# Performance work log

Hardware: AMD Instinct MI355X
Metric: run time of the kernel (lower is better)

The kernel has to match this reference:

```python
import jax, jax.numpy as jnp
import numpy as np

DIM = 1024
HEADS = 16
DH = 64            # dim // heads
LOCAL_HEADS = 8
WINDOW = 128
NEG = -jnp.finfo(jnp.float32).max


def _look_around_kv(z, pad_value):
    # z: (b, h, nw, w, d) -> (b, h, nw, 3w, d); backward=1, forward=1 window
    nw = z.shape[2]
    zp = jnp.pad(z, ((0, 0), (0, 0), (1, 1), (0, 0), (0, 0)), constant_values=pad_value)
    return jnp.concatenate([zp[:, :, i:i + nw] for i in range(3)], axis=3)


def _local_attention(q, k, v, valid):
    # q,k,v: (b, h, t, d); valid: (b, t) True = keep (module passes ~input_mask)
    b, h, t, d = q.shape
    nw = t // WINDOW
    bucket = lambda z: z.reshape(b, h, nw, WINDOW, d)
    bq, bk, bv = bucket(q), bucket(k), bucket(v)
    bk = _look_around_kv(bk, 0.0)
    bv = _look_around_kv(bv, 0.0)
    # key position indices with -1 padding for out-of-range windows
    t_idx = jnp.arange(t, dtype=jnp.int32).reshape(nw, WINDOW)
    tp = jnp.pad(t_idx, ((1, 1), (0, 0)), constant_values=-1)
    bq_k = jnp.concatenate([tp[i:i + nw] for i in range(3)], axis=1)  # (nw, 3w)
    oob = (bq_k == -1)[None, None, :, None, :]                        # (1,1,nw,1,3w)
    # input mask pair: mq & mk
    vm = valid.reshape(b, nw, WINDOW)
    vmp = jnp.pad(vm, ((0, 0), (1, 1), (0, 0)), constant_values=False)
    vmk = jnp.concatenate([vmp[:, i:i + nw] for i in range(3)], axis=2)  # (b, nw, 3w)
    pair = vm[:, None, :, :, None] & vmk[:, None, :, None, :]            # (b,1,nw,w,3w)
    dots = jnp.einsum('bhnwd,bhnkd->bhnwk', bq, bk) * (d ** -0.5)
    dots = jnp.where(oob, NEG, dots)
    dots = jnp.where(pair, dots, NEG)
    attn = jax.nn.softmax(dots, axis=-1)
    out = jnp.einsum('bhnwk,bhnkd->bhnwd', attn, bv)
    return out.reshape(b, h, t, d)


def _linear_attn(q, k, v, valid):
    # q,k,v: (b, h, t, d); valid: (b, t) True = keep
    d = q.shape[-1]
    m = valid[:, None, :, None]
    k = jnp.where(m, k, NEG)
    v = jnp.where(m, v, 0.0)
    q = jax.nn.softmax(q, axis=-1) * (d ** -0.5)
    k = jax.nn.softmax(k, axis=-2)
    context = jnp.einsum('bhnd,bhne->bhde', k, v)
    return jnp.einsum('bhnd,bhde->bhne', q, context)


def setup_inputs() -> dict:
    key = jax.random.key(0)
    ks = jax.random.split(key, 7)
    b, t = 2, 4096
    x = jax.random.normal(ks[0], (b, t, DIM), dtype=jnp.float32)
    input_mask = jax.random.bernoulli(ks[1], 0.1, (b, t))  # True = padded token
    s = DIM ** -0.5
    Wq = jax.random.normal(ks[2], (DIM, HEADS * DH), jnp.float32) * s
    Wk = jax.random.normal(ks[3], (DIM, HEADS * DH), jnp.float32) * s
    Wv = jax.random.normal(ks[4], (DIM, HEADS * DH), jnp.float32) * s
    Wo = jax.random.normal(ks[5], (HEADS * DH, DIM), jnp.float32) * s
    bo = jax.random.normal(ks[6], (DIM,), jnp.float32) * 0.01
    return {"x": x, "input_mask": input_mask, "Wq": Wq, "Wk": Wk, "Wv": Wv, "Wo": Wo, "bo": bo}


def reference(x, input_mask, Wq, Wk, Wv, Wo, bo):
    b, t, _ = x.shape
    split_heads = lambda z: z.reshape(b, t, HEADS, DH).transpose(0, 2, 1, 3)
    q = split_heads(x @ Wq)
    k = split_heads(x @ Wk)
    v = split_heads(x @ Wv)
    valid = ~input_mask
    lq, gq = q[:, :LOCAL_HEADS], q[:, LOCAL_HEADS:]
    lk, gk = k[:, :LOCAL_HEADS], k[:, LOCAL_HEADS:]
    lv, gv = v[:, :LOCAL_HEADS], v[:, LOCAL_HEADS:]
    local_out = _local_attention(lq, lk, lv, valid)
    global_out = _linear_attn(gq, gk, gv, valid)
    attn = jnp.concatenate([local_out, global_out], axis=1)  # (b, h, t, d)
    attn = attn.transpose(0, 2, 1, 3).reshape(b, t, HEADS * DH)
    return attn @ Wo + bo
```

## Files before the change

### kernel.cpp

```cpp
#include <hip/hip_runtime.h>
#include <cstdint>
#include <cfloat>
#include <math.h>

typedef __bf16 bf16_t;
typedef __bf16 bf16x8 __attribute__((ext_vector_type(8)));
typedef __bf16 bf16x4 __attribute__((ext_vector_type(4)));
typedef float  f32x4  __attribute__((ext_vector_type(4)));
typedef unsigned int u32;

#define NEGF (-3.4028234663852886e38f)

static __device__ __forceinline__ f32x4 mfma16(bf16x8 a, bf16x8 b, f32x4 c) {
  return __builtin_amdgcn_mfma_f32_16x16x32_bf16(a, b, c, 0, 0, 0);
}
static __device__ __forceinline__ void gload_lds16(const bf16_t* g, bf16_t* l) {
  __builtin_amdgcn_global_load_lds((const __attribute__((address_space(1))) void*)g,
                                   (__attribute__((address_space(3))) void*)l, 16, 0, 0);
}

__global__ __launch_bounds__(256) void k_prep_all(const float* __restrict__ x,
                                                  const uint8_t* __restrict__ mraw,
                                                  const float* __restrict__ Wq,
                                                  const float* __restrict__ Wk,
                                                  const float* __restrict__ Wv,
                                                  const float* __restrict__ Wo,
                                                  bf16_t* __restrict__ xb,
                                                  bf16_t* __restrict__ WT,
                                                  bf16_t* __restrict__ WoT,
                                                  uint8_t* __restrict__ valid) {
  int bid = blockIdx.x;
  int tid = threadIdx.x;
  if (bid < 8192) {
    int i = bid * 256 + tid;
    float4 v = ((const float4*)x)[i];
    bf16x4 o = { (bf16_t)v.x, (bf16_t)v.y, (bf16_t)v.z, (bf16_t)v.w };
    *(bf16x4*)(xb + (size_t)i * 4) = o;
  } else if (bid < 12288) {
    __shared__ float tile[32][33];
    int zz = bid - 8192;
    int z = zz >> 10, rem = zz & 1023;
    int bx = rem & 31, by = rem >> 5;
    const float* src = (z == 0) ? Wq : (z == 1) ? Wk : (z == 2) ? Wv : Wo;
    bf16_t* dst = (z < 3) ? (WT + (size_t)z * 1024 * 1024) : WoT;
    int x0 = bx * 32, y0 = by * 32;
    int tx = tid & 31, ty = tid >> 5;
    #pragma unroll
    for (int j = 0; j < 32; j += 8)
      tile[ty + j][tx] = src[(size_t)(y0 + ty + j) * 1024 + x0 + tx];
    __syncthreads();
    #pragma unroll
    for (int j = 0; j < 32; j += 8)
      dst[(size_t)(x0 + ty + j) * 1024 + y0 + tx] = (bf16_t)tile[tx][ty + j];
  } else {
    __shared__ int f1, f3;
    if (tid == 0) { f1 = 0; f3 = 0; }
    __syncthreads();
    int l1 = 0, l3 = 0;
    for (int i = tid; i < 8192; i += 256) {
      uint8_t v = mraw[i];
      if (v) { int r = i & 3; if (r == 1 || r == 2) l1 = 1; if (r == 3) l3 = 1; }
    }
    if (l1) atomicOr(&f1, 1);
    if (l3) atomicOr(&f3, 1);
    __syncthreads();
    int layout = f1 ? 0 : (f3 ? 2 : 1);
    for (int i = tid; i < 8192; i += 256) {
      bool m;
      if (layout == 0)      m = mraw[i] != 0;
      else if (layout == 1) m = ((const int*)mraw)[i] != 0;
      else                  m = ((const float*)mraw)[i] != 0.0f;
      valid[i] = m ? (uint8_t)0 : (uint8_t)1;
    }
  }
}

template<bool OUT_BF16>
__global__ __launch_bounds__(256, 2) void k_gemm(const bf16_t* __restrict__ A,
                                                 const bf16_t* __restrict__ Bt,
                                                 void* __restrict__ Cout,
                                                 const float* __restrict__ bias,
                                                 int M, int N, int K) {
  __shared__ __align__(16) uint8_t shmem[34816];
  bf16_t* As = (bf16_t*)shmem;
  bf16_t* Bs = As + 128 * 64;
  int id  = blockIdx.x;
  int seq = id >> 3;
  int nbg = seq >> 6, inner = seq & 63;
  int mb = ((id & 7) << 3) + (inner >> 3);
  int nb = (nbg << 3) + (inner & 7);

  const int tid = threadIdx.x;
  const int lane = tid & 63, wv = tid >> 6;
  const int c = lane & 15, g = lane >> 4;
  const size_t m0 = (size_t)mb * 128, n0 = (size_t)nb * 128;
  const int wm = (wv >> 1) * 64, wn = (wv & 1) * 64;

  f32x4 zero = {0.f, 0.f, 0.f, 0.f};
  f32x4 acc[4][4];
  #pragma unroll
  for (int m = 0; m < 4; ++m)
    #pragma unroll
    for (int n = 0; n < 4; ++n) acc[m][n] = zero;

  for (int kt = 0; kt < K; kt += 64) {
    if (kt) __syncthreads();
    #pragma unroll
    for (int p = 0; p < 4; ++p) {
      int seg = p * 256 + tid;
      int r = seg >> 3, s = seg & 7;
      int sc = (s ^ (r & 7)) * 8;
      gload_lds16(A + (m0 + r) * (size_t)K + kt + sc, As + seg * 8);
    }
    #pragma unroll
    for (int p = 0; p < 4; ++p) {
      int seg = p * 256 + tid;
      int r = seg >> 3, s = seg & 7;
      int sc = (s ^ (r & 7)) * 8;
      gload_lds16(Bt + (n0 + r) * (size_t)K + kt + sc, Bs + seg * 8);
    }
    __syncthreads();
    #pragma unroll
    for (int kk = 0; kk < 2; ++kk) {
      bf16x8 af[4], bfv[4];
      #pragma unroll
      for (int m = 0; m < 4; ++m) {
        int row = wm + m * 16 + c;
        int sl = (g + 4 * kk) ^ (row & 7);
        af[m] = *(const bf16x8*)(As + row * 64 + sl * 8);
      }
      #pragma unroll
      for (int n = 0; n < 4; ++n) {
        int row = wn + n * 16 + c;
        int sl = (g + 4 * kk) ^ (row & 7);
        bfv[n] = *(const bf16x8*)(Bs + row * 64 + sl * 8);
      }
      #pragma unroll
      for (int m = 0; m < 4; ++m)
        #pragma unroll
        for (int n = 0; n < 4; ++n)
          acc[m][n] = mfma16(af[m], bfv[n], acc[m][n]);
    }
  }

  __syncthreads();
  if (OUT_BF16) {
    bf16_t* L = (bf16_t*)shmem;
    #pragma unroll
    for (int m = 0; m < 4; ++m)
      #pragma unroll
      for (int n = 0; n < 4; ++n)
        #pragma unroll
        for (int i = 0; i < 4; ++i)
          L[(wm + m * 16 + 4 * g + i) * 136 + wn + n * 16 + c] = (bf16_t)acc[m][n][i];
    __syncthreads();
    bf16_t* C = (bf16_t*)Cout;
    #pragma unroll
    for (int p = 0; p < 8; ++p) {
      int idx = p * 2048 + tid * 8;
      int row = idx >> 7, col = idx & 127;
      bf16x8 v = *(const bf16x8*)(L + row * 136 + col);
      *(bf16x8*)(C + (m0 + row) * (size_t)N + n0 + col) = v;
    }
  } else {
    float* C = (float*)Cout;
    float* L = (float*)shmem;
    #pragma unroll
    for (int half = 0; half < 2; ++half) {
      if (half) __syncthreads();
      if ((wv >> 1) == half) {
        #pragma unroll
        for (int m = 0; m < 4; ++m)
          #pragma unroll
          for (int n = 0; n < 4; ++n)
            #pragma unroll
            for (int i = 0; i < 4; ++i)
              L[(m * 16 + 4 * g + i) * 132 + wn + n * 16 + c] = acc[m][n][i];
      }
      __syncthreads();
      #pragma unroll
      for (int p = 0; p < 8; ++p) {
        int lin = p * 1024 + tid * 4;
        int row = lin >> 7, col = lin & 127;
        float4 v = *(const float4*)(L + row * 132 + col);
        float4 bv = *(const float4*)(bias + n0 + col);
        v.x += bv.x; v.y += bv.y; v.z += bv.z; v.w += bv.w;
        *(float4*)(C + (m0 + half * 64 + row) * (size_t)N + n0 + col) = v;
      }
    }
  }
}

__global__ __launch_bounds__(512) void k_attn(const bf16_t* __restrict__ qkv,
                                              const uint8_t* __restrict__ valid,
                                              bf16_t* __restrict__ attn,
                                              float* __restrict__ ctxp,
                                              float* __restrict__ sump) {
  __shared__ __align__(16) uint8_t smem[50688];
  int bid = blockIdx.x;
  int tid = threadIdx.x;
  const int lane = tid & 63, wv = tid >> 6;
  const int c = lane & 15, g = lane >> 4;
  f32x4 zero = {0.f, 0.f, 0.f, 0.f};

  if (bid < 512) {
    bf16_t* Ks = (bf16_t*)smem;
    bf16_t* VT = (bf16_t*)smem;
    uint8_t* s_key = smem + 50176;
    uint8_t* s_q   = smem + 50560;

    int w = bid & 31, h = (bid >> 5) & 7, b = bid >> 8;
    const int tkbase = (w - 1) * 128;

    #pragma unroll
    for (int p = 0; p < 6; ++p) {
      int seg = p * 512 + tid;
      int r = seg >> 3, s = seg & 7;
      int tk = tkbase + r;
      bf16x8 v8 = { (bf16_t)0.f,(bf16_t)0.f,(bf16_t)0.f,(bf16_t)0.f,
                    (bf16_t)0.f,(bf16_t)0.f,(bf16_t)0.f,(bf16_t)0.f };
      if ((unsigned)tk < 4096u)
        v8 = *(const bf16x8*)(qkv + (size_t)(b * 4096 + tk) * 3072 + 1024 + h * 64 + s * 8);
      *(bf16x8*)(Ks + r * 64 + ((s ^ (r & 7)) * 8)) = v8;
    }
    if (tid < 384) {
      int tk = tkbase + tid;
      s_key[tid] = ((unsigned)tk < 4096u) ? valid[b * 4096 + tk] : (uint8_t)0;
    }
    if (tid < 128) s_q[tid] = valid[b * 4096 + w * 128 + tid];
    __syncthreads();

    int m0 = wv * 16;
    bf16x8 qa0, qa1;
    {
      const bf16_t* qrow = qkv + (size_t)(b * 4096 + w * 128 + m0 + c) * 3072 + h * 64;
      qa0 = *(const bf16x8*)(qrow + g * 8);
      qa1 = *(const bf16x8*)(qrow + 32 + g * 8);
    }
    f32x4 acc[24];
    #pragma unroll
    for (int nt = 0; nt < 24; ++nt) acc[nt] = zero;
    #pragma unroll
    for (int nt = 0; nt < 24; ++nt) {
      int n = nt * 16 + c;
      bf16x8 k0 = *(const bf16x8*)(Ks + n * 64 + ((g       ^ (n & 7)) * 8));
      bf16x8 k1 = *(const bf16x8*)(Ks + n * 64 + (((g + 4) ^ (n & 7)) * 8));
      acc[nt] = mfma16(k0, qa0, acc[nt]);
      acc[nt] = mfma16(k1, qa1, acc[nt]);
    }
    __syncthreads();

    #pragma unroll
    for (int p = 0; p < 6; ++p) {
      int seg = p * 512 + tid;
      int r = seg >> 3, s = seg & 7;
      int tk = tkbase + r;
      bf16x8 v8 = { (bf16_t)0.f,(bf16_t)0.f,(bf16_t)0.f,(bf16_t)0.f,
                    (bf16_t)0.f,(bf16_t)0.f,(bf16_t)0.f,(bf16_t)0.f };
      if ((unsigned)tk < 4096u)
        v8 = *(const bf16x8*)(qkv + (size_t)(b * 4096 + tk) * 3072 + 2048 + h * 64 + s * 8);
      #pragma unroll
      for (int j = 0; j < 8; ++j)
        VT[(s * 8 + j) * 392 + r] = v8[j];
    }

    bool qv = s_q[m0 + c] != 0;
    #pragma unroll
    for (int nt = 0; nt < 24; ++nt) {
      u32 kv4 = *(const u32*)(s_key + nt * 16 + 4 * g);
      #pragma unroll
      for (int i = 0; i < 4; ++i) {
        bool kv = ((kv4 >> (8 * i)) & 255u) != 0u;
        acc[nt][i] = (qv && kv) ? acc[nt][i] * 0.125f : NEGF;
      }
    }
    float mx = NEGF;
    #pragma unroll
    for (int nt = 0; nt < 24; ++nt)
      #pragma unroll
      for (int i = 0; i < 4; ++i) mx = fmaxf(mx, acc[nt][i]);
    mx = fmaxf(mx, __shfl_xor(mx, 16, 64));
    mx = fmaxf(mx, __shfl_xor(mx, 32, 64));

    const int srcA = ((lane >> 4) & 1) * 32 + (lane & 15);
    const int srcB = srcA + 16;
    union Pk2 { bf16x4 h; uint2 u; };
    union Pk4 { uint4 u; bf16x8 h; };
    uint4 paU[12];
    #pragma unroll
    for (int ks = 0; ks < 12; ++ks) paU[ks] = make_uint4(0, 0, 0, 0);
    float sum = 0.f;
    #pragma unroll
    for (int nt = 0; nt < 24; ++nt) {
      Pk2 pk;
      #pragma unroll
      for (int i = 0; i < 4; ++i) {
        float e = __expf(acc[nt][i] - mx);
        sum += e;
        pk.h[i] = (bf16_t)e;
      }
      u32 a0 = (u32)__shfl((int)pk.u.x, srcA, 64);
      u32 a1 = (u32)__shfl((int)pk.u.y, srcA, 64);
      u32 b0 = (u32)__shfl((int)pk.u.x, srcB, 64);
      u32 b1 = (u32)__shfl((int)pk.u.y, srcB, 64);
      bool take = ((g >> 1) == (nt & 1));
      int ks = nt >> 1;
      paU[ks].x = take ? a0 : paU[ks].x;
      paU[ks].y = take ? a1 : paU[ks].y;
      paU[ks].z = take ? b0 : paU[ks].z;
      paU[ks].w = take ? b1 : paU[ks].w;
    }
    sum += __shfl_xor(sum, 16, 64);
    sum += __shfl_xor(sum, 32, 64);
    float inv = 1.f / sum;
    float invq[4];
    #pragma unroll
    for (int i = 0; i < 4; ++i) invq[i] = __shfl(inv, 4 * g + i, 64);
    __syncthreads();

    f32x4 o[4];
    #pragma unroll
    for (int n = 0; n < 4; ++n) o[n] = zero;
    #pragma unroll
    for (int ks = 0; ks < 12; ++ks) {
      Pk4 pa; pa.u = paU[ks];
      #pragma unroll
      for (int n = 0; n < 4; ++n) {
        bf16x8 vb = *(const bf16x8*)(VT + (n * 16 + c) * 392 + ks * 32 + g * 8);
        o[n] = mfma16(pa.h, vb, o[n]);
      }
    }
    size_t obase = (size_t)(b * 4096 + w * 128 + m0) * 1024 + h * 64;
    #pragma unroll
    for (int n = 0; n < 4; ++n)
      #pragma unroll
      for (int i = 0; i < 4; ++i)
        attn[obase + (size_t)(4 * g + i) * 1024 + n * 16 + c] = (bf16_t)(o[n][i] * invq[i]);
  } else {
    int bid2 = bid - 512;
    int tc = bid2 & 15, h = (bid2 >> 4) & 7, b = bid2 >> 7;
    bf16_t* eKT = (bf16_t*)smem;
    bf16_t* vT  = (bf16_t*)(smem + 17408);
    int dt = wv >> 1, et2 = (wv & 1) * 2;
    f32x4 acc2[2];
    acc2[0] = zero; acc2[1] = zero;
    float rowsum = 0.f;
    int rsrow = wv * 8 + (lane >> 3);
    int rscol = (lane & 7) * 16;
    for (int ch = 0; ch < 2; ++ch) {
      __syncthreads();
      #pragma unroll
      for (int p = 0; p < 2; ++p) {
        int idx = p * 512 + tid;
        int r = idx >> 3, ss = idx & 7;
        int gt = b * 4096 + tc * 256 + ch * 128 + r;
        bool vld = valid[gt] != 0;
        bf16x8 k8 = *(const bf16x8*)(qkv + (size_t)gt * 3072 + 1024 + (8 + h) * 64 + ss * 8);
        bf16x8 v8 = *(const bf16x8*)(qkv + (size_t)gt * 3072 + 2048 + (8 + h) * 64 + ss * 8);
        #pragma unroll
        for (int j = 0; j < 8; ++j) {
          int dd = ss * 8 + j;
          eKT[dd * 136 + r] = vld ? (bf16_t)__expf((float)k8[j]) : (bf16_t)0.f;
          vT [dd * 136 + r] = vld ? v8[j] : (bf16_t)0.f;
        }
      }
      __syncthreads();
      #pragma unroll
      for (int ks = 0; ks < 4; ++ks) {
        bf16x8 af = *(const bf16x8*)(eKT + (dt * 16 + c) * 136 + ks * 32 + g * 8);
        #pragma unroll
        for (int n = 0; n < 2; ++n) {
          bf16x8 bf = *(const bf16x8*)(vT + ((et2 + n) * 16 + c) * 136 + ks * 32 + g * 8);
          acc2[n] = mfma16(af, bf, acc2[n]);
        }
      }
      float s = 0.f;
      #pragma unroll
      for (int q = 0; q < 2; ++q) {
        bf16x8 e8 = *(const bf16x8*)(eKT + rsrow * 136 + rscol + q * 8);
        #pragma unroll
        for (int j = 0; j < 8; ++j) s += (float)e8[j];
      }
      rowsum += s;
    }
    rowsum += __shfl_xor(rowsum, 1, 64);
    rowsum += __shfl_xor(rowsum, 2, 64);
    rowsum += __shfl_xor(rowsum, 4, 64);
    size_t slice = (size_t)((b * 8 + h) * 16 + tc);
    #pragma unroll
    for (int n = 0; n < 2; ++n)
      #pragma unroll
      for (int i = 0; i < 4; ++i)
        ctxp[slice * 4096 + (size_t)(dt * 16 + 4 * g + i) * 64 + (et2 + n) * 16 + c] = acc2[n][i];
    if ((lane & 7) == 0)
      sump[slice * 64 + rsrow] = rowsum;
  }
}

__global__ __launch_bounds__(256) void k_ctx2(const float* __restrict__ ctxp,
                                              const float* __restrict__ sump,
                                              bf16_t* __restrict__ ctxT) {
  int bh = blockIdx.x;
  int tid = threadIdx.x;
  __shared__ float inv[64];
  if (tid < 64) {
    float s = 0.f;
    #pragma unroll
    for (int tc = 0; tc < 16; ++tc)
      s += sump[(size_t)(bh * 16 + tc) * 64 + tid];
    inv[tid] = 1.f / s;
  }
  __syncthreads();
  for (int p = 0; p < 16; ++p) {
    int lin = p * 256 + tid;
    int d = lin >> 6, e = lin & 63;
    float s = 0.f;
    #pragma unroll
    for (int tc = 0; tc < 16; ++tc)
      s += ctxp[(size_t)(bh * 16 + tc) * 4096 + lin];
    s *= inv[d];
    ctxT[(size_t)bh * 4096 + e * 64 + d] = (bf16_t)s;
  }
}

__global__ __launch_bounds__(256) void k_linout(const bf16_t* __restrict__ qkv,
                                                const bf16_t* __restrict__ ctxT,
                                                bf16_t* __restrict__ attn) {
  int bid = blockIdx.x;
  int tb2 = bid & 15, hg = (bid >> 4) & 7, b = bid >> 7;
  int tid = threadIdx.x;
  __shared__ bf16_t qs[256 * 72];
  __shared__ bf16_t cT[64 * 72];
  {
    int t = tb2 * 256 + tid;
    const bf16_t* qrow = qkv + (size_t)(b * 4096 + t) * 3072 + (8 + hg) * 64;
    float x[64];
    #pragma unroll
    for (int s8 = 0; s8 < 8; ++s8) {
      bf16x8 q8 = *(const bf16x8*)(qrow + s8 * 8);
      #pragma unroll
      for (int j = 0; j < 8; ++j) x[s8 * 8 + j] = (float)q8[j];
    }
    float m = x[0];
    #pragma unroll
    for (int i = 1; i < 64; ++i) m = fmaxf(m, x[i]);
    float sum = 0.f;
    #pragma unroll
    for (int i = 0; i < 64; ++i) { x[i] = __expf(x[i] - m); sum += x[i]; }
    float sc = 0.125f / sum;
    #pragma unroll
    for (int s8 = 0; s8 < 8; ++s8) {
      bf16x8 o8;
      #pragma unroll
      for (int j = 0; j < 8; ++j) o8[j] = (bf16_t)(x[s8 * 8 + j] * sc);
      *(bf16x8*)(qs + tid * 72 + s8 * 8) = o8;
    }
  }
  for (int idx = tid; idx < 512; idx += 256) {
    int r = idx >> 3, s = idx & 7;
    *(bf16x8*)(cT + r * 72 + s * 8) =
      *(const bf16x8*)(ctxT + (size_t)(b * 8 + hg) * 4096 + r * 64 + s * 8);
  }
  __syncthreads();
  int lane = tid & 63, wvv = tid >> 6;
  int c = lane & 15, g = lane >> 4;
  int m0w = wvv * 64;
  f32x4 zero = {0.f, 0.f, 0.f, 0.f};
  f32x4 acc[4][4];
  #pragma unroll
  for (int m = 0; m < 4; ++m)
    #pragma unroll
    for (int n = 0; n < 4; ++n) acc[m][n] = zero;
  #pragma unroll
  for (int kk = 0; kk < 2; ++kk) {
    bf16x8 af[4], bfv[4];
    #pragma unroll
    for (int m = 0; m < 4; ++m)
      af[m] = *(const bf16x8*)(qs + (m0w + m * 16 + c) * 72 + kk * 32 + g * 8);
    #pragma unroll
    for (int n = 0; n < 4; ++n)
      bfv[n] = *(const bf16x8*)(cT + (n * 16 + c) * 72 + kk * 32 + g * 8);
    #pragma unroll
    for (int m = 0; m < 4; ++m)
      #pragma unroll
      for (int n = 0; n < 4; ++n)
        acc[m][n] = mfma16(af[m], bfv[n], acc[m][n]);
  }
  size_t obase = (size_t)(b * 4096 + tb2 * 256 + m0w) * 1024 + (8 + hg) * 64;
  #pragma unroll
  for (int m = 0; m < 4; ++m)
    #pragma unroll
    for (int n = 0; n < 4; ++n)
      #pragma unroll
      for (int i = 0; i < 4; ++i)
        attn[obase + (size_t)(m * 16 + 4 * g + i) * 1024 + n * 16 + c] = (bf16_t)acc[m][n][i];
}

extern "C" void kernel_launch(void* const* d_in, const int* in_sizes, int n_in,
                              void* d_out, int out_size, void* d_ws, size_t ws_size,
                              hipStream_t stream) {
  const float*   x    = (const float*)d_in[0];
  const uint8_t* mraw = (const uint8_t*)d_in[1];
  const float*   Wq   = (const float*)d_in[2];
  const float*   Wk   = (const float*)d_in[3];
  const float*   Wv   = (const float*)d_in[4];
  const float*   Wo   = (const float*)d_in[5];
  const float*   bo   = (const float*)d_in[6];
  uint8_t* ws = (uint8_t*)d_ws;

  uint8_t* valid = ws;
  bf16_t*  xb    = (bf16_t*)(ws + 8192);
  bf16_t*  WT    = (bf16_t*)(ws + 16785408);
  bf16_t*  WoT   = (bf16_t*)(ws + 23076864);
  bf16_t*  qkv   = (bf16_t*)(ws + 25174016);
  bf16_t*  attn  = (bf16_t*)(ws + 75505664);
  float*   ctxp  = (float*)(ws + 8192);
  float*   sump  = (float*)(ws + 4202496);
  bf16_t*  ctxT  = (bf16_t*)(ws + 4268032);

  k_prep_all<<<12289, 256, 0, stream>>>(x, mraw, Wq, Wk, Wv, Wo, xb, WT, WoT, valid);
  k_gemm<true><<<1536, 256, 0, stream>>>(xb, WT, (void*)qkv, nullptr, 8192, 3072, 1024);
  k_attn<<<768, 512, 0, stream>>>(qkv, valid, attn, ctxp, sump);
  k_ctx2<<<16, 256, 0, stream>>>(ctxp, sump, ctxT);
  k_linout<<<256, 256, 0, stream>>>(qkv, ctxT, attn);
  k_gemm<false><<<512, 256, 0, stream>>>(attn, WoT, d_out, bo, 8192, 1024, 1024);
}
```

Before: 177.0 us.

## Overlap K/V global loads with compute via direct-to-LDS and register prefetch

In the local-attention blocks, K is now staged with direct global-to-LDS loads in the same XOR-swizzled layout. V is loaded into registers during the QK^T/softmax phase and only transposed into LDS after softmax, which removes a barrier. In the linear-attention blocks, the two-chunk loop is unrolled so the second chunk's K/V global loads are issued before the first chunk's MFMA work. The K load drops the bounds check, so edge windows read rows outside the valid range; those scores are masked later, but the reads could land outside the buffer, and register pressure goes up.

```diff
diff --git a/kernel.cpp b/kernel.cpp
--- a/kernel.cpp
+++ b/kernel.cpp
@@ -211,32 +211,30 @@
 
     int w = bid & 31, h = (bid >> 5) & 7, b = bid >> 8;
     const int tkbase = (w - 1) * 128;
-
-    #pragma unroll
-    for (int p = 0; p < 6; ++p) {
-      int seg = p * 512 + tid;
-      int r = seg >> 3, s = seg & 7;
-      int tk = tkbase + r;
-      bf16x8 v8 = { (bf16_t)0.f,(bf16_t)0.f,(bf16_t)0.f,(bf16_t)0.f,
-                    (bf16_t)0.f,(bf16_t)0.f,(bf16_t)0.f,(bf16_t)0.f };
-      if ((unsigned)tk < 4096u)
-        v8 = *(const bf16x8*)(qkv + (size_t)(b * 4096 + tk) * 3072 + 1024 + h * 64 + s * 8);
-      *(bf16x8*)(Ks + r * 64 + ((s ^ (r & 7)) * 8)) = v8;
-    }
-    if (tid < 384) {
-      int tk = tkbase + tid;
-      s_key[tid] = ((unsigned)tk < 4096u) ? valid[b * 4096 + tk] : (uint8_t)0;
-    }
-    if (tid < 128) s_q[tid] = valid[b * 4096 + w * 128 + tid];
-    __syncthreads();
-
     int m0 = wv * 16;
+
     bf16x8 qa0, qa1;
     {
       const bf16_t* qrow = qkv + (size_t)(b * 4096 + w * 128 + m0 + c) * 3072 + h * 64;
       qa0 = *(const bf16x8*)(qrow + g * 8);
       qa1 = *(const bf16x8*)(qrow + 32 + g * 8);
     }
+
+    #pragma unroll
+    for (int p = 0; p < 6; ++p) {
+      int seg = p * 512 + tid;
+      int r = seg >> 3, s = seg & 7;
+      int sc = (s ^ (r & 7)) * 8;
+      gload_lds16(qkv + (size_t)(b * 4096 + tkbase + r) * 3072 + 1024 + h * 64 + sc,
+                  Ks + seg * 8);
+    }
+    if (tid < 384) {
+      int tk = tkbase + tid;
+      s_key[tid] = ((unsigned)tk < 4096u) ? valid[b * 4096 + tk] : (uint8_t)0;
+    }
+    if (tid < 128) s_q[tid] = valid[b * 4096 + w * 128 + tid];
+    __syncthreads();
+
     f32x4 acc[24];
     #pragma unroll
     for (int nt = 0; nt < 24; ++nt) acc[nt] = zero;
@@ -248,8 +246,8 @@
       acc[nt] = mfma16(k0, qa0, acc[nt]);
       acc[nt] = mfma16(k1, qa1, acc[nt]);
     }
-    __syncthreads();
-
+
+    bf16x8 vreg[6];
     #pragma unroll
     for (int p = 0; p < 6; ++p) {
       int seg = p * 512 + tid;
@@ -259,10 +257,9 @@
                     (bf16_t)0.f,(bf16_t)0.f,(bf16_t)0.f,(bf16_t)0.f };
       if ((unsigned)tk < 4096u)
         v8 = *(const bf16x8*)(qkv + (size_t)(b * 4096 + tk) * 3072 + 2048 + h * 64 + s * 8);
-      #pragma unroll
-      for (int j = 0; j < 8; ++j)
-        VT[(s * 8 + j) * 392 + r] = v8[j];
-    }
+      vreg[p] = v8;
+    }
+    __syncthreads();
 
     bool qv = s_q[m0 + c] != 0;
     #pragma unroll
@@ -316,6 +313,15 @@
     float invq[4];
     #pragma unroll
     for (int i = 0; i < 4; ++i) invq[i] = __shfl(inv, 4 * g + i, 64);
+
+    #pragma unroll
+    for (int p = 0; p < 6; ++p) {
+      int seg = p * 512 + tid;
+      int r = seg >> 3, s = seg & 7;
+      #pragma unroll
+      for (int j = 0; j < 8; ++j)
+        VT[(s * 8 + j) * 392 + r] = vreg[p][j];
+    }
     __syncthreads();
 
     f32x4 o[4];
@@ -347,33 +353,81 @@
     float rowsum = 0.f;
     int rsrow = wv * 8 + (lane >> 3);
     int rscol = (lane & 7) * 16;
-    for (int ch = 0; ch < 2; ++ch) {
-      __syncthreads();
-      #pragma unroll
-      for (int p = 0; p < 2; ++p) {
-        int idx = p * 512 + tid;
-        int r = idx >> 3, ss = idx & 7;
-        int gt = b * 4096 + tc * 256 + ch * 128 + r;
-        bool vld = valid[gt] != 0;
-        bf16x8 k8 = *(const bf16x8*)(qkv + (size_t)gt * 3072 + 1024 + (8 + h) * 64 + ss * 8);
-        bf16x8 v8 = *(const bf16x8*)(qkv + (size_t)gt * 3072 + 2048 + (8 + h) * 64 + ss * 8);
+    int r0 = tid >> 3, ss0 = tid & 7;
+    int r1 = (512 + tid) >> 3, ss1 = tid & 7;
+
+    bf16x8 k8a[2], v8a[2]; bool vldA[2];
+    #pragma unroll
+    for (int p = 0; p < 2; ++p) {
+      int r = (p == 0) ? r0 : r1;
+      int gt = b * 4096 + tc * 256 + r;
+      vldA[p] = valid[gt] != 0;
+      k8a[p] = *(const bf16x8*)(qkv + (size_t)gt * 3072 + 1024 + (8 + h) * 64 + ss0 * 8);
+      v8a[p] = *(const bf16x8*)(qkv + (size_t)gt * 3072 + 2048 + (8 + h) * 64 + ss0 * 8);
+    }
+    #pragma unroll
+    for (int p = 0; p < 2; ++p) {
+      int r = (p == 0) ? r0 : r1;
+      int rr = r & 127;
+      #pragma unroll
+      for (int j = 0; j < 8; ++j) {
+        int dd = ss0 * 8 + j;
+        eKT[dd * 136 + rr] = vldA[p] ? (bf16_t)__expf((float)k8a[p][j]) : (bf16_t)0.f;
+        vT [dd * 136 + rr] = vldA[p] ? v8a[p][j] : (bf16_t)0.f;
+      }
+    }
+    bf16x8 k8b[2], v8b[2]; bool vldB[2];
+    #pragma unroll
+    for (int p = 0; p < 2; ++p) {
+      int r = (p == 0) ? r0 : r1;
+      int gt = b * 4096 + tc * 256 + 128 + r;
+      vldB[p] = valid[gt] != 0;
+      k8b[p] = *(const bf16x8*)(qkv + (size_t)gt * 3072 + 1024 + (8 + h) * 64 + ss0 * 8);
+      v8b[p] = *(const bf16x8*)(qkv + (size_t)gt * 3072 + 2048 + (8 + h) * 64 + ss0 * 8);
+    }
+    __syncthreads();
+    #pragma unroll
+    for (int ks = 0; ks < 4; ++ks) {
+      bf16x8 af = *(const bf16x8*)(eKT + (dt * 16 + c) * 136 + ks * 32 + g * 8);
+      #pragma unroll
+      for (int n = 0; n < 2; ++n) {
+        bf16x8 bf = *(const bf16x8*)(vT + ((et2 + n) * 16 + c) * 136 + ks * 32 + g * 8);
+        acc2[n] = mfma16(af, bf, acc2[n]);
+      }
+    }
+    {
+      float s = 0.f;
+      #pragma unroll
+      for (int q = 0; q < 2; ++q) {
+        bf16x8 e8 = *(const bf16x8*)(eKT + rsrow * 136 + rscol + q * 8);
         #pragma unroll
-        for (int j = 0; j < 8; ++j) {
-          int dd = ss * 8 + j;
-          eKT[dd * 136 + r] = vld ? (bf16_t)__expf((float)k8[j]) : (bf16_t)0.f;
-          vT [dd * 136 + r] = vld ? v8[j] : (bf16_t)0.f;
-        }
-      }
-      __syncthreads();
-      #pragma unroll
-      for (int ks = 0; ks < 4; ++ks) {
-        bf16x8 af = *(const bf16x8*)(eKT + (dt * 16 + c) * 136 + ks * 32 + g * 8);
-        #pragma unroll
-        for (int n = 0; n < 2; ++n) {
-          bf16x8 bf = *(const bf16x8*)(vT + ((et2 + n) * 16 + c) * 136 + ks * 32 + g * 8);
-          acc2[n] = mfma16(af, bf, acc2[n]);
-        }
-      }
+        for (int j = 0; j < 8; ++j) s += (float)e8[j];
+      }
+      rowsum += s;
+    }
+    __syncthreads();
+    #pragma unroll
+    for (int p = 0; p < 2; ++p) {
+      int r = (p == 0) ? r0 : r1;
+      int rr = r & 127;
+      #pragma unroll
+      for (int j = 0; j < 8; ++j) {
+        int dd = ss0 * 8 + j;
+        eKT[dd * 136 + rr] = vldB[p] ? (bf16_t)__expf((float)k8b[p][j]) : (bf16_t)0.f;
+        vT [dd * 136 + rr] = vldB[p] ? v8b[p][j] : (bf16_t)0.f;
+      }
+    }
+    __syncthreads();
+    #pragma unroll
+    for (int ks = 0; ks < 4; ++ks) {
+      bf16x8 af = *(const bf16x8*)(eKT + (dt * 16 + c) * 136 + ks * 32 + g * 8);
+      #pragma unroll
+      for (int n = 0; n < 2; ++n) {
+        bf16x8 bf = *(const bf16x8*)(vT + ((et2 + n) * 16 + c) * 136 + ks * 32 + g * 8);
+        acc2[n] = mfma16(af, bf, acc2[n]);
+      }
+    }
+    {
       float s = 0.f;
       #pragma unroll
       for (int q = 0; q < 2; ++q) {
```

Result: slower. 182.1 us (+2.9%).

## Replace QKV projection GEMM with 256x128-tile 8-wave ping-pong pipelined kernel

Applied to the files above, without the earlier changes.

Adds a new bf16 GEMM kernel for the QKV projection. It uses 512 threads, a 256x128 output tile and double-buffered LDS staged through global_load_lds. Compute is split into four MFMA phases that interleave the next tile's loads, with barriers and s_setprio raising MFMA priority. The output goes through LDS for coalesced stores. The aim is to hide global-load latency and raise MFMA utilisation compared with the old 128-tile kernel, at the cost of a large 96KB LDS footprint and lower occupancy.

```diff
diff --git a/kernel.cpp b/kernel.cpp
--- a/kernel.cpp
+++ b/kernel.cpp
@@ -75,6 +75,169 @@
   }
 }
 
+__global__ __launch_bounds__(512) void k_gemm8p(const bf16_t* __restrict__ A,
+                                                const bf16_t* __restrict__ Bt,
+                                                bf16_t* __restrict__ C,
+                                                int M, int N, int K) {
+  __shared__ __align__(16) uint8_t shmem[98304];
+  bf16_t* lds = (bf16_t*)shmem;
+  const int NT = K >> 6;
+  int id = blockIdx.x;
+  int xcd = id & 7, seq = id >> 3;
+  int nbg = seq >> 5, inner = seq & 31;
+  int mb = (xcd << 2) + (inner >> 3);
+  int nb = (nbg << 3) + (inner & 7);
+
+  const int tid = threadIdx.x;
+  const int lane = tid & 63, wv = tid >> 6;
+  const int c = lane & 15, g = lane >> 4;
+  const size_t m0 = (size_t)mb * 256, n0 = (size_t)nb * 128;
+  const int wm = (wv >> 1) * 64, wn = (wv & 1) * 64;
+
+  auto stageA = [&](int t, int half) {
+    #pragma unroll
+    for (int p = 0; p < 2; ++p) {
+      int seg = half * 1024 + p * 512 + tid;
+      int r = seg >> 3, s = seg & 7;
+      int sc = (s ^ (r & 7)) * 8;
+      gload_lds16(A + (m0 + r) * (size_t)K + (t << 6) + sc,
+                  lds + (t & 1) * 24576 + seg * 8);
+    }
+  };
+  auto stageB = [&](int t) {
+    #pragma unroll
+    for (int p = 0; p < 2; ++p) {
+      int seg = p * 512 + tid;
+      int r = seg >> 3, s = seg & 7;
+      int sc = (s ^ (r & 7)) * 8;
+      gload_lds16(Bt + (n0 + r) * (size_t)K + (t << 6) + sc,
+                  lds + (t & 1) * 24576 + 16384 + seg * 8);
+    }
+  };
+
+  f32x4 zero = {0.f, 0.f, 0.f, 0.f};
+  f32x4 acc[4][4];
+  #pragma unroll
+  for (int m = 0; m < 4; ++m)
+    #pragma unroll
+    for (int n = 0; n < 4; ++n) acc[m][n] = zero;
+
+  stageA(0, 0); stageA(0, 1); stageB(0);
+  asm volatile("s_waitcnt vmcnt(0)" ::: "memory");
+  __builtin_amdgcn_s_barrier();
+
+  for (int t = 0; t < NT; ++t) {
+    const bf16_t* As = lds + (t & 1) * 24576;
+    const bf16_t* Bs = As + 16384;
+    bool pf = (t + 1) < NT;
+    bf16x8 bA[2][2], bB[4][2];
+
+    #pragma unroll
+    for (int m = 0; m < 2; ++m) {
+      int row = wm + m * 16 + c;
+      bA[m][0] = *(const bf16x8*)(As + row * 64 + ((g       ^ (row & 7)) * 8));
+      bA[m][1] = *(const bf16x8*)(As + row * 64 + (((g + 4) ^ (row & 7)) * 8));
+    }
+    #pragma unroll
+    for (int n = 0; n < 2; ++n) {
+      int row = wn + n * 16 + c;
+      bB[n][0] = *(const bf16x8*)(Bs + row * 64 + ((g       ^ (row & 7)) * 8));
+      bB[n][1] = *(const bf16x8*)(Bs + row * 64 + (((g + 4) ^ (row & 7)) * 8));
+    }
+    if (pf) stageA(t + 1, 0);
+    __builtin_amdgcn_s_barrier();
+    asm volatile("s_waitcnt lgkmcnt(0)" ::: "memory");
+    __builtin_amdgcn_sched_barrier(0);
+    __builtin_amdgcn_s_setprio(1);
+    #pragma unroll
+    for (int m = 0; m < 2; ++m)
+      #pragma unroll
+      for (int n = 0; n < 2; ++n) {
+        acc[m][n] = mfma16(bA[m][0], bB[n][0], acc[m][n]);
+        acc[m][n] = mfma16(bA[m][1], bB[n][1], acc[m][n]);
+      }
+    __builtin_amdgcn_s_setprio(0);
+    __builtin_amdgcn_s_barrier();
+
+    #pragma unroll
+    for (int n = 2; n < 4; ++n) {
+      int row = wn + n * 16 + c;
+      bB[n][0] = *(const bf16x8*)(Bs + row * 64 + ((g       ^ (row & 7)) * 8));
+      bB[n][1] = *(const bf16x8*)(Bs + row * 64 + (((g + 4) ^ (row & 7)) * 8));
+    }
+    if (pf) stageA(t + 1, 1);
+    __builtin_amdgcn_s_barrier();
+    asm volatile("s_waitcnt lgkmcnt(0)" ::: "memory");
+    __builtin_amdgcn_sched_barrier(0);
+    __builtin_amdgcn_s_setprio(1);
+    #pragma unroll
+    for (int m = 0; m < 2; ++m)
+      #pragma unroll
+      for (int n = 2; n < 4; ++n) {
+        acc[m][n] = mfma16(bA[m][0], bB[n][0], acc[m][n]);
+        acc[m][n] = mfma16(bA[m][1], bB[n][1], acc[m][n]);
+      }
+    __builtin_amdgcn_s_setprio(0);
+    __builtin_amdgcn_s_barrier();
+
+    #pragma unroll
+    for (int m = 0; m < 2; ++m) {
+      int row = wm + (m + 2) * 16 + c;
+      bA[m][0] = *(const bf16x8*)(As + row * 64 + ((g       ^ (row & 7)) * 8));
+      bA[m][1] = *(const bf16x8*)(As + row * 64 + (((g + 4) ^ (row & 7)) * 8));
+    }
+    if (pf) stageB(t + 1);
+    __builtin_amdgcn_s_barrier();
+    asm volatile("s_waitcnt lgkmcnt(0)" ::: "memory");
+    __builtin_amdgcn_sched_barrier(0);
+    __builtin_amdgcn_s_setprio(1);
+    #pragma unroll
+    for (int m = 0; m < 2; ++m)
+      #pragma unroll
+      for (int n = 0; n < 2; ++n) {
+        acc[m + 2][n] = mfma16(bA[m][0], bB[n][0], acc[m + 2][n]);
+        acc[m + 2][n] = mfma16(bA[m][1], bB[n][1], acc[m + 2][n]);
+      }
+    __builtin_amdgcn_s_setprio(0);
+    __builtin_amdgcn_s_barrier();
+
+    __builtin_amdgcn_s_setprio(1);
+    #pragma unroll
+    for (int m = 0; m < 2; ++m)
+      #pragma unroll
+      for (int n = 2; n < 4; ++n) {
+        acc[m + 2][n] = mfma16(bA[m][0], bB[n][0], acc[m + 2][n]);
+        acc[m + 2][n] = mfma16(bA[m][1], bB[n][1], acc[m + 2][n]);
+      }
+    __builtin_amdgcn_s_setprio(0);
+
+    if (pf) {
+      asm volatile("s_waitcnt vmcnt(0)" ::: "memory");
+      __builtin_amdgcn_s_barrier();
+    }
+  }
+
+  __syncthreads();
+  {
+    bf16_t* L = (bf16_t*)shmem;
+    #pragma unroll
+    for (int m = 0; m < 4; ++m)
+      #pragma unroll
+      for (int n = 0; n < 4; ++n)
+        #pragma unroll
+        for (int i = 0; i < 4; ++i)
+          L[(wm + m * 16 + 4 * g + i) * 136 + wn + n * 16 + c] = (bf16_t)acc[m][n][i];
+    __syncthreads();
+    #pragma unroll
+    for (int p = 0; p < 8; ++p) {
+      int idx = p * 4096 + tid * 8;
+      int row = idx >> 7, col = idx & 127;
+      bf16x8 v = *(const bf16x8*)(L + row * 136 + col);
+      *(bf16x8*)(C + (m0 + row) * (size_t)N + n0 + col) = v;
+    }
+  }
+}
+
 template<bool OUT_BF16>
 __global__ __launch_bounds__(256, 2) void k_gemm(const bf16_t* __restrict__ A,
                                                  const bf16_t* __restrict__ Bt,
@@ -519,7 +682,7 @@
   bf16_t*  ctxT  = (bf16_t*)(ws + 4268032);
 
   k_prep_all<<<12289, 256, 0, stream>>>(x, mraw, Wq, Wk, Wv, Wo, xb, WT, WoT, valid);
-  k_gemm<true><<<1536, 256, 0, stream>>>(xb, WT, (void*)qkv, nullptr, 8192, 3072, 1024);
+  k_gemm8p<<<768, 512, 0, stream>>>(xb, WT, qkv, 8192, 3072, 1024);
   k_attn<<<768, 512, 0, stream>>>(qkv, valid, attn, ctxp, sump);
   k_ctx2<<<16, 256, 0, stream>>>(ctxp, sump, ctxT);
   k_linout<<<256, 256, 0, stream>>>(qkv, ctxT, attn);
```

Measured after the change: 188.4 us. 6.5% more time.
